# Kernel tuning notes

Measured on AMD Instinct MI355X. Metric: run time of the kernel, lower is better.

## Reference

```python
import jax, jax.numpy as jnp
import numpy as np

N = 4096        # n_nodes; must equal HID due to the model's mean(dim=1)->classifier quirk
IN_DIM = 512
HID = 4096
E = 65536       # N * avg_degree(16)


def _lin(k, out_dim, in_dim):
    return jax.random.normal(k, (out_dim, in_dim), jnp.float32) * 0.02


def setup_inputs() -> dict:
    key = jax.random.key(0)
    ks = jax.random.split(key, 8)
    return {
        "x": jax.random.normal(ks[0], (N, IN_DIM), jnp.float32),
        "edge_index": jax.random.randint(ks[1], (2, E), 0, N, dtype=jnp.int32),
        "W_embed": _lin(ks[2], HID, IN_DIM),
        "b_embed": jnp.zeros((HID,), jnp.float32),
        "W1": _lin(ks[3], HID, HID),
        "b1": jnp.zeros((HID,), jnp.float32),
        "W2": _lin(ks[4], HID, HID),
        "b2": jnp.zeros((HID,), jnp.float32),
        "Wc1": _lin(ks[5], HID // 2, HID),
        "bc1": jnp.zeros((HID // 2,), jnp.float32),
        "Wc2": _lin(ks[6], 1, HID // 2),
        "bc2": jnp.zeros((1,), jnp.float32),
    }


def reference(x, edge_index, W_embed, b_embed, W1, b1, W2, b2, Wc1, bc1, Wc2, bc2):
    row, col = edge_index[0], edge_index[1]
    # embed: Linear(in_dim, hidden)
    h = x @ W_embed.T + b_embed                       # [N, HID]
    # two GNN layers: gather neighbors, scatter-add, linear + relu
    for W, b in ((W1, b1), (W2, b2)):
        aggr = jax.ops.segment_sum(h[col], row, num_segments=h.shape[0])  # [N, HID]
        h = jax.nn.relu(aggr @ W.T + b)
    # faithful to original: mean over feature dim -> [N] (N == HID)
    hm = jnp.mean(h, axis=1)                          # [HID]
    z = jax.nn.relu(hm @ Wc1.T + bc1)                 # [HID//2]
    out = (z @ Wc2.T + bc2).squeeze(-1)               # scalar
    return out
```

## Files before the change

### kernel.cpp

```cpp
#include <hip/hip_runtime.h>
#include <hip/hip_bf16.h>


#define N_NODES 4096
#define IN_DIM_ 512
#define HID_ 4096
#define NEDGE 65536

typedef float f32x4 __attribute__((ext_vector_type(4)));
typedef float f32x2 __attribute__((ext_vector_type(2)));
typedef unsigned short u16x8 __attribute__((ext_vector_type(8)));
typedef int i32x8 __attribute__((ext_vector_type(8)));

#define ACT_SCALE 8.0f
#define W_SCALE 256.0f
#define G_SCALE 8.0f
#define G_STORE_MUL (8.0f / 2048.0f)

__device__ __forceinline__ unsigned short f2bf(float f) {
  unsigned u = __float_as_uint(f);
  return (unsigned short)((u + 0x7fffu + ((u >> 16) & 1u)) >> 16);
}
__device__ __forceinline__ float bf2f(unsigned short h) {
  return __uint_as_float((unsigned)h << 16);
}
__device__ __forceinline__ unsigned char f2fp8(float f) {
  int w = __builtin_amdgcn_cvt_pk_fp8_f32(f, f, 0, false);
  return (unsigned char)(w & 0xff);
}
__device__ __forceinline__ void fp8x4_acc(int w, float* acc) {
  f32x2 lo = __builtin_amdgcn_cvt_pk_f32_fp8(w, false);
  f32x2 hi = __builtin_amdgcn_cvt_pk_f32_fp8(w, true);
  acc[0] += lo[0]; acc[1] += lo[1]; acc[2] += hi[0]; acc[3] += hi[1];
}

__global__ __launch_bounds__(256) void cvt_fp8(const float* __restrict__ in,
                                               unsigned char* __restrict__ out,
                                               int n, float scale) {
  int i = (blockIdx.x * 256 + threadIdx.x) * 8;
  if (i >= n) return;
  const float4 a = *(const float4*)(in + i);
  const float4 b = *(const float4*)(in + i + 4);
  int w0 = __builtin_amdgcn_cvt_pk_fp8_f32(a.x * scale, a.y * scale, 0, false);
  w0 = __builtin_amdgcn_cvt_pk_fp8_f32(a.z * scale, a.w * scale, w0, true);
  int w1 = __builtin_amdgcn_cvt_pk_fp8_f32(b.x * scale, b.y * scale, 0, false);
  w1 = __builtin_amdgcn_cvt_pk_fp8_f32(b.z * scale, b.w * scale, w1, true);
  *(int2*)(out + i) = make_int2(w0, w1);
}

__global__ __launch_bounds__(256) void zero_i32(int* __restrict__ p, int n) {
  int i = blockIdx.x * 256 + threadIdx.x;
  if (i < n) p[i] = 0;
}

__global__ __launch_bounds__(256) void hist_rows(const int* __restrict__ row,
                                                 int* __restrict__ counts) {
  int e = blockIdx.x * 256 + threadIdx.x;
  if (e < NEDGE) atomicAdd(&counts[row[e]], 1);
}

__global__ __launch_bounds__(1024) void scan4096(const int* __restrict__ counts,
                                                 int* __restrict__ starts) {
  __shared__ int sa[1024], sb[1024];
  const int t = threadIdx.x;
  const int c0 = counts[t * 4], c1 = counts[t * 4 + 1],
            c2 = counts[t * 4 + 2], c3 = counts[t * 4 + 3];
  const int local = c0 + c1 + c2 + c3;
  sa[t] = local;
  __syncthreads();
  int* src = sa; int* dst = sb;
  for (int off = 1; off < 1024; off <<= 1) {
    int v = src[t];
    if (t >= off) v += src[t - off];
    dst[t] = v;
    __syncthreads();
    int* tmp = src; src = dst; dst = tmp;
  }
  const int excl = (t == 0) ? 0 : src[t - 1];
  starts[t * 4]     = excl;
  starts[t * 4 + 1] = excl + c0;
  starts[t * 4 + 2] = excl + c0 + c1;
  starts[t * 4 + 3] = excl + c0 + c1 + c2;
  if (t == 1023) starts[4096] = excl + local;
}

__global__ __launch_bounds__(256) void fill_adj(const int* __restrict__ row,
                                                const int* __restrict__ col,
                                                const int* __restrict__ starts,
                                                int* __restrict__ cursor,
                                                int* __restrict__ adj) {
  int e = blockIdx.x * 256 + threadIdx.x;
  if (e >= NEDGE) return;
  int r = row[e];
  int p = atomicAdd(&cursor[r], 1);
  adj[starts[r] + p] = col[e];
}

__device__ __forceinline__ i32x8 ld_frag(const char* base0) {
  const int4 lo = *(const int4*)(base0);
  const int4 hi = *(const int4*)(base0 + 8192);
  i32x8 f;
  f[0] = lo.x; f[1] = lo.y; f[2] = lo.z; f[3] = lo.w;
  f[4] = hi.x; f[5] = hi.y; f[6] = hi.z; f[7] = hi.w;
  return f;
}

__global__ __launch_bounds__(256) void gemm_mx(
    const unsigned char* __restrict__ A, const unsigned char* __restrict__ B,
    unsigned char* __restrict__ C, int N, int K,
    const float* __restrict__ bias, float mul) {
  __shared__ unsigned char As[128 * 128];
  __shared__ unsigned char Bs[128 * 128];
  const int t = threadIdx.x;
  const int bm = blockIdx.x * 128, bn = blockIdx.y * 128;
  const int wave = t >> 6, lane = t & 63;
  const int wm = (wave >> 1) * 64, wn = (wave & 1) * 64;
  const int m16 = lane & 15, quad = lane >> 4;

  f32x4 acc[4][4] = {};

  const int srow = t >> 2;
  const int sg = (t & 3) * 32;
  const unsigned char* Ag0 = A + (size_t)(bm + srow) * K + sg;
  const unsigned char* Ag1 = A + (size_t)(bm + 64 + srow) * K + sg;
  const unsigned char* Bg0 = B + (size_t)(bn + srow) * K + sg;
  const unsigned char* Bg1 = B + (size_t)(bn + 64 + srow) * K + sg;
  char* AsB = (char*)As;
  char* BsB = (char*)Bs;

#define GLDS(gp, lp)                                                       \
  __builtin_amdgcn_global_load_lds(                                        \
      (const __attribute__((address_space(1))) void*)(gp),                 \
      (__attribute__((address_space(3))) void*)(lp), 16, 0, 0)

  for (int kb = 0; kb < K; kb += 128) {
    GLDS(Ag0 + kb,      AsB + t * 16);
    GLDS(Ag1 + kb,      AsB + 4096 + t * 16);
    GLDS(Ag0 + kb + 16, AsB + 8192 + t * 16);
    GLDS(Ag1 + kb + 16, AsB + 12288 + t * 16);
    GLDS(Bg0 + kb,      BsB + t * 16);
    GLDS(Bg1 + kb,      BsB + 4096 + t * 16);
    GLDS(Bg0 + kb + 16, BsB + 8192 + t * 16);
    GLDS(Bg1 + kb + 16, BsB + 12288 + t * 16);
    __syncthreads();

    i32x8 af[4], bfr[4];
#pragma unroll
    for (int r = 0; r < 4; ++r)
      af[r] = ld_frag(AsB + (wm + r * 16 + m16) * 64 + quad * 16);
#pragma unroll
    for (int c = 0; c < 4; ++c)
      bfr[c] = ld_frag(BsB + (wn + c * 16 + m16) * 64 + quad * 16);
#pragma unroll
    for (int r = 0; r < 4; ++r)
#pragma unroll
      for (int c = 0; c < 4; ++c)
        acc[r][c] = __builtin_amdgcn_mfma_scale_f32_16x16x128_f8f6f4(
            af[r], bfr[c], acc[r][c], 0, 0,
            0, 0x7f7f7f7f, 0, 0x7f7f7f7f);
    __syncthreads();
  }
#undef GLDS

#pragma unroll
  for (int r = 0; r < 4; ++r) {
#pragma unroll
    for (int c = 0; c < 4; ++c) {
      const int row0 = bm + wm + r * 16 + quad * 4;
      const int col = bn + wn + c * 16 + m16;
      const float bv = bias ? ACT_SCALE * bias[col] : 0.0f;
#pragma unroll
      for (int i = 0; i < 4; ++i) {
        C[(size_t)(row0 + i) * N + col] = f2fp8(acc[r][c][i] * mul + bv);
      }
    }
  }
}

__global__ __launch_bounds__(256) void aggr_f8out(
    const unsigned char* __restrict__ g, const int* __restrict__ starts,
    const int* __restrict__ adj, const float* __restrict__ bias,
    unsigned char* __restrict__ hout) {
  const int node = blockIdx.y;
  const int f0 = blockIdx.x * 2048 + threadIdx.x * 8;
  float acc[8] = {0, 0, 0, 0, 0, 0, 0, 0};
  const int s = starts[node], e = starts[node + 1];
  int j = s;
  for (; j + 4 <= e; j += 4) {
    const int c0 = adj[j], c1 = adj[j + 1], c2 = adj[j + 2], c3 = adj[j + 3];
    int2 v0 = *(const int2*)(g + (size_t)c0 * HID_ + f0);
    int2 v1 = *(const int2*)(g + (size_t)c1 * HID_ + f0);
    int2 v2 = *(const int2*)(g + (size_t)c2 * HID_ + f0);
    int2 v3 = *(const int2*)(g + (size_t)c3 * HID_ + f0);
    fp8x4_acc(v0.x, acc);     fp8x4_acc(v0.y, acc + 4);
    fp8x4_acc(v1.x, acc);     fp8x4_acc(v1.y, acc + 4);
    fp8x4_acc(v2.x, acc);     fp8x4_acc(v2.y, acc + 4);
    fp8x4_acc(v3.x, acc);     fp8x4_acc(v3.y, acc + 4);
  }
  for (; j < e; ++j) {
    int2 v = *(const int2*)(g + (size_t)adj[j] * HID_ + f0);
    fp8x4_acc(v.x, acc);      fp8x4_acc(v.y, acc + 4);
  }
  const float4 b0 = *(const float4*)(bias + f0);
  const float4 b1 = *(const float4*)(bias + f0 + 4);
  const float bb[8] = {b0.x, b0.y, b0.z, b0.w, b1.x, b1.y, b1.z, b1.w};
  float v[8];
#pragma unroll
  for (int i = 0; i < 8; ++i)
    v[i] = ACT_SCALE * fmaxf(acc[i] * (1.0f / G_SCALE) + bb[i], 0.0f);
  int w0 = __builtin_amdgcn_cvt_pk_fp8_f32(v[0], v[1], 0, false);
  w0 = __builtin_amdgcn_cvt_pk_fp8_f32(v[2], v[3], w0, true);
  int w1 = __builtin_amdgcn_cvt_pk_fp8_f32(v[4], v[5], 0, false);
  w1 = __builtin_amdgcn_cvt_pk_fp8_f32(v[6], v[7], w1, true);
  *(int2*)(hout + (size_t)node * HID_ + f0) = make_int2(w0, w1);
}

__global__ __launch_bounds__(256) void aggr_bf16out(
    const unsigned char* __restrict__ g, const int* __restrict__ starts,
    const int* __restrict__ adj, const float* __restrict__ bias,
    unsigned short* __restrict__ hout) {
  const int node = blockIdx.y;
  const int f0 = blockIdx.x * 2048 + threadIdx.x * 8;
  float acc[8] = {0, 0, 0, 0, 0, 0, 0, 0};
  const int s = starts[node], e = starts[node + 1];
  int j = s;
  for (; j + 4 <= e; j += 4) {
    const int c0 = adj[j], c1 = adj[j + 1], c2 = adj[j + 2], c3 = adj[j + 3];
    int2 v0 = *(const int2*)(g + (size_t)c0 * HID_ + f0);
    int2 v1 = *(const int2*)(g + (size_t)c1 * HID_ + f0);
    int2 v2 = *(const int2*)(g + (size_t)c2 * HID_ + f0);
    int2 v3 = *(const int2*)(g + (size_t)c3 * HID_ + f0);
    fp8x4_acc(v0.x, acc);     fp8x4_acc(v0.y, acc + 4);
    fp8x4_acc(v1.x, acc);     fp8x4_acc(v1.y, acc + 4);
    fp8x4_acc(v2.x, acc);     fp8x4_acc(v2.y, acc + 4);
    fp8x4_acc(v3.x, acc);     fp8x4_acc(v3.y, acc + 4);
  }
  for (; j < e; ++j) {
    int2 v = *(const int2*)(g + (size_t)adj[j] * HID_ + f0);
    fp8x4_acc(v.x, acc);      fp8x4_acc(v.y, acc + 4);
  }
  const float4 b0 = *(const float4*)(bias + f0);
  const float4 b1 = *(const float4*)(bias + f0 + 4);
  const float bb[8] = {b0.x, b0.y, b0.z, b0.w, b1.x, b1.y, b1.z, b1.w};
  u16x8 r;
#pragma unroll
  for (int i = 0; i < 8; ++i)
    r[i] = f2bf(fmaxf(acc[i] * (1.0f / G_SCALE) + bb[i], 0.0f));
  *(u16x8*)(hout + (size_t)node * HID_ + f0) = r;
}

__global__ __launch_bounds__(256) void row_mean(const unsigned short* __restrict__ h,
                                                float* __restrict__ hm) {
  const int row = blockIdx.x, t = threadIdx.x;
  const u16x8* p = (const u16x8*)(h + (size_t)row * HID_);
  u16x8 v1 = p[t], v2 = p[t + 256];
  float s = 0.f;
#pragma unroll
  for (int i = 0; i < 8; ++i) s += bf2f(v1[i]) + bf2f(v2[i]);
  for (int off = 32; off > 0; off >>= 1) s += __shfl_down(s, off);
  __shared__ float ws[4];
  if ((t & 63) == 0) ws[t >> 6] = s;
  __syncthreads();
  if (t == 0) hm[row] = (ws[0] + ws[1] + ws[2] + ws[3]) * (1.0f / (float)HID_);
}

__global__ __launch_bounds__(256) void clf1(const float* __restrict__ Wc1,
                                            const float* __restrict__ bc1,
                                            const float* __restrict__ hm,
                                            float* __restrict__ z) {
  const int wave = threadIdx.x >> 6, lane = threadIdx.x & 63;
  const int j = blockIdx.x * 4 + wave;
  const float* w = Wc1 + (size_t)j * HID_;
  float s = 0.f;
  for (int i = lane; i < HID_; i += 64) s += w[i] * hm[i];
  for (int off = 32; off > 0; off >>= 1) s += __shfl_down(s, off);
  if (lane == 0) z[j] = fmaxf(s + bc1[j], 0.0f);
}

__global__ __launch_bounds__(256) void clf2(const float* __restrict__ Wc2,
                                            const float* __restrict__ bc2,
                                            const float* __restrict__ z,
                                            float* __restrict__ out) {
  const int t = threadIdx.x;
  float s = 0.f;
  for (int i = t; i < HID_ / 2; i += 256) s += z[i] * Wc2[i];
  for (int off = 32; off > 0; off >>= 1) s += __shfl_down(s, off);
  __shared__ float ws[4];
  if ((t & 63) == 0) ws[t >> 6] = s;
  __syncthreads();
  if (t == 0) out[0] = ws[0] + ws[1] + ws[2] + ws[3] + bc2[0];
}

extern "C" void kernel_launch(void* const* d_in, const int* in_sizes, int n_in,
                              void* d_out, int out_size, void* d_ws, size_t ws_size,
                              hipStream_t stream) {
  (void)in_sizes; (void)n_in; (void)out_size; (void)ws_size;
  const float* x       = (const float*)d_in[0];
  const int*   edge    = (const int*)d_in[1];
  const int*   row     = edge;
  const int*   col     = edge + NEDGE;
  const float* W_embed = (const float*)d_in[2];
  const float* b_embed = (const float*)d_in[3];
  const float* W1      = (const float*)d_in[4];
  const float* b1      = (const float*)d_in[5];
  const float* W2      = (const float*)d_in[6];
  const float* b2      = (const float*)d_in[7];
  const float* Wc1     = (const float*)d_in[8];
  const float* bc1     = (const float*)d_in[9];
  const float* Wc2     = (const float*)d_in[10];
  const float* bc2     = (const float*)d_in[11];
  float* out = (float*)d_out;

  char* ws = (char*)d_ws;
  size_t off = 0;
  auto alloc = [&](size_t bytes) {
    char* p = ws + off;
    off += (bytes + 255) & ~(size_t)255;
    return p;
  };
  unsigned char*  xf8  = (unsigned char*)alloc((size_t)N_NODES * IN_DIM_);
  unsigned char*  wef8 = (unsigned char*)alloc((size_t)HID_ * IN_DIM_);
  unsigned char*  w1f8 = (unsigned char*)alloc((size_t)HID_ * HID_);
  unsigned char*  w2f8 = (unsigned char*)alloc((size_t)HID_ * HID_);
  unsigned char*  h0f8 = (unsigned char*)alloc((size_t)N_NODES * HID_);
  unsigned char*  h1f8 = (unsigned char*)alloc((size_t)N_NODES * HID_);
  unsigned char*  g    = (unsigned char*)alloc((size_t)N_NODES * HID_);
  unsigned short* h2   = (unsigned short*)alloc((size_t)N_NODES * HID_ * 2);
  int* counts = (int*)alloc(N_NODES * 4);
  int* cursor = (int*)alloc(N_NODES * 4);
  int* starts = (int*)alloc((N_NODES + 1) * 4);
  int* adj    = (int*)alloc(NEDGE * 4);
  float* hm   = (float*)alloc(N_NODES * 4);
  float* z    = (float*)alloc((HID_ / 2) * 4);

  zero_i32<<<16, 256, 0, stream>>>(counts, N_NODES);
  zero_i32<<<16, 256, 0, stream>>>(cursor, N_NODES);
  hist_rows<<<NEDGE / 256, 256, 0, stream>>>(row, counts);
  scan4096<<<1, 1024, 0, stream>>>(counts, starts);
  fill_adj<<<NEDGE / 256, 256, 0, stream>>>(row, col, starts, cursor, adj);

  cvt_fp8<<<(N_NODES * IN_DIM_ / 8) / 256, 256, 0, stream>>>(x, xf8, N_NODES * IN_DIM_, ACT_SCALE);
  cvt_fp8<<<(HID_ * IN_DIM_ / 8) / 256, 256, 0, stream>>>(W_embed, wef8, HID_ * IN_DIM_, W_SCALE);
  cvt_fp8<<<(HID_ * HID_ / 8) / 256, 256, 0, stream>>>(W1, w1f8, HID_ * HID_, W_SCALE);
  cvt_fp8<<<(HID_ * HID_ / 8) / 256, 256, 0, stream>>>(W2, w2f8, HID_ * HID_, W_SCALE);

  gemm_mx<<<dim3(32, 32), 256, 0, stream>>>(xf8, wef8, h0f8, HID_, IN_DIM_,
                                            b_embed, G_STORE_MUL);
  gemm_mx<<<dim3(32, 32), 256, 0, stream>>>(h0f8, w1f8, g, HID_, HID_,
                                            nullptr, G_STORE_MUL);
  aggr_f8out<<<dim3(2, N_NODES), 256, 0, stream>>>(g, starts, adj, b1, h1f8);
  gemm_mx<<<dim3(32, 32), 256, 0, stream>>>(h1f8, w2f8, g, HID_, HID_,
                                            nullptr, G_STORE_MUL);
  aggr_bf16out<<<dim3(2, N_NODES), 256, 0, stream>>>(g, starts, adj, b2, h2);
  row_mean<<<N_NODES, 256, 0, stream>>>(h2, hm);
  clf1<<<(HID_ / 2) / 4, 256, 0, stream>>>(Wc1, bc1, hm, z);
  clf2<<<1, 256, 0, stream>>>(Wc2, bc2, z, out);
}
```

Baseline: 483.3 us.

## Fuse row-mean into second aggregation, merge conversions, classifiers, and zeroing

The second aggregation now reduces each node's ReLU output directly into the row mean with an atomicAdd, so the bf16 h2 buffer and the separate row_mean kernel are no longer needed. The four fp8 conversion launches become one, the two zeroing launches become one (it also clears hm and the output), and the two classifier kernels are fused by atomically accumulating z*Wc2 into the output. This cuts launch count and removes the write and re-read of a 32MB intermediate. In exchange, float atomics make the summation order nondeterministic.

```diff
diff --git a/kernel.cpp b/kernel.cpp
--- a/kernel.cpp
+++ b/kernel.cpp
@@ -9,7 +9,6 @@
 
 typedef float f32x4 __attribute__((ext_vector_type(4)));
 typedef float f32x2 __attribute__((ext_vector_type(2)));
-typedef unsigned short u16x8 __attribute__((ext_vector_type(8)));
 typedef int i32x8 __attribute__((ext_vector_type(8)));
 
 #define ACT_SCALE 8.0f
@@ -17,13 +16,6 @@
 #define G_SCALE 8.0f
 #define G_STORE_MUL (8.0f / 2048.0f)
 
-__device__ __forceinline__ unsigned short f2bf(float f) {
-  unsigned u = __float_as_uint(f);
-  return (unsigned short)((u + 0x7fffu + ((u >> 16) & 1u)) >> 16);
-}
-__device__ __forceinline__ float bf2f(unsigned short h) {
-  return __uint_as_float((unsigned)h << 16);
-}
 __device__ __forceinline__ unsigned char f2fp8(float f) {
   int w = __builtin_amdgcn_cvt_pk_fp8_f32(f, f, 0, false);
   return (unsigned char)(w & 0xff);
@@ -34,23 +26,32 @@
   acc[0] += lo[0]; acc[1] += lo[1]; acc[2] += hi[0]; acc[3] += hi[1];
 }
 
-__global__ __launch_bounds__(256) void cvt_fp8(const float* __restrict__ in,
-                                               unsigned char* __restrict__ out,
-                                               int n, float scale) {
-  int i = (blockIdx.x * 256 + threadIdx.x) * 8;
-  if (i >= n) return;
+__global__ __launch_bounds__(256) void zero_misc(int* __restrict__ p, int n,
+                                                 float* __restrict__ out) {
+  int i = blockIdx.x * 256 + threadIdx.x;
+  if (i < n) p[i] = 0;
+  if (i == 0) out[0] = 0.0f;
+}
+
+__global__ __launch_bounds__(256) void cvt_all(
+    const float* __restrict__ x, const float* __restrict__ we,
+    const float* __restrict__ w1, const float* __restrict__ w2,
+    unsigned char* __restrict__ xo, unsigned char* __restrict__ weo,
+    unsigned char* __restrict__ w1o, unsigned char* __restrict__ w2o) {
+  const int b = blockIdx.x;
+  const float* in; unsigned char* out; float scale; int base;
+  if (b < 1024)       { in = x;  out = xo;  scale = ACT_SCALE; base = b; }
+  else if (b < 2048)  { in = we; out = weo; scale = W_SCALE;   base = b - 1024; }
+  else if (b < 10240) { in = w1; out = w1o; scale = W_SCALE;   base = b - 2048; }
+  else                { in = w2; out = w2o; scale = W_SCALE;   base = b - 10240; }
+  const int i = (base * 256 + threadIdx.x) * 8;
   const float4 a = *(const float4*)(in + i);
-  const float4 b = *(const float4*)(in + i + 4);
+  const float4 c = *(const float4*)(in + i + 4);
   int w0 = __builtin_amdgcn_cvt_pk_fp8_f32(a.x * scale, a.y * scale, 0, false);
   w0 = __builtin_amdgcn_cvt_pk_fp8_f32(a.z * scale, a.w * scale, w0, true);
-  int w1 = __builtin_amdgcn_cvt_pk_fp8_f32(b.x * scale, b.y * scale, 0, false);
-  w1 = __builtin_amdgcn_cvt_pk_fp8_f32(b.z * scale, b.w * scale, w1, true);
-  *(int2*)(out + i) = make_int2(w0, w1);
-}
-
-__global__ __launch_bounds__(256) void zero_i32(int* __restrict__ p, int n) {
-  int i = blockIdx.x * 256 + threadIdx.x;
-  if (i < n) p[i] = 0;
+  int w1v = __builtin_amdgcn_cvt_pk_fp8_f32(c.x * scale, c.y * scale, 0, false);
+  w1v = __builtin_amdgcn_cvt_pk_fp8_f32(c.z * scale, c.w * scale, w1v, true);
+  *(int2*)(out + i) = make_int2(w0, w1v);
 }
 
 __global__ __launch_bounds__(256) void hist_rows(const int* __restrict__ row,
@@ -215,10 +216,10 @@
   *(int2*)(hout + (size_t)node * HID_ + f0) = make_int2(w0, w1);
 }
 
-__global__ __launch_bounds__(256) void aggr_bf16out(
+__global__ __launch_bounds__(256) void aggr_mean(
     const unsigned char* __restrict__ g, const int* __restrict__ starts,
     const int* __restrict__ adj, const float* __restrict__ bias,
-    unsigned short* __restrict__ hout) {
+    float* __restrict__ hm) {
   const int node = blockIdx.y;
   const int f0 = blockIdx.x * 2048 + threadIdx.x * 8;
   float acc[8] = {0, 0, 0, 0, 0, 0, 0, 0};
@@ -242,53 +243,35 @@
   const float4 b0 = *(const float4*)(bias + f0);
   const float4 b1 = *(const float4*)(bias + f0 + 4);
   const float bb[8] = {b0.x, b0.y, b0.z, b0.w, b1.x, b1.y, b1.z, b1.w};
-  u16x8 r;
+  float s8 = 0.f;
 #pragma unroll
   for (int i = 0; i < 8; ++i)
-    r[i] = f2bf(fmaxf(acc[i] * (1.0f / G_SCALE) + bb[i], 0.0f));
-  *(u16x8*)(hout + (size_t)node * HID_ + f0) = r;
-}
-
-__global__ __launch_bounds__(256) void row_mean(const unsigned short* __restrict__ h,
-                                                float* __restrict__ hm) {
-  const int row = blockIdx.x, t = threadIdx.x;
-  const u16x8* p = (const u16x8*)(h + (size_t)row * HID_);
-  u16x8 v1 = p[t], v2 = p[t + 256];
-  float s = 0.f;
-#pragma unroll
-  for (int i = 0; i < 8; ++i) s += bf2f(v1[i]) + bf2f(v2[i]);
-  for (int off = 32; off > 0; off >>= 1) s += __shfl_down(s, off);
+    s8 += fmaxf(acc[i] * (1.0f / G_SCALE) + bb[i], 0.0f);
+  for (int off = 32; off > 0; off >>= 1) s8 += __shfl_down(s8, off);
   __shared__ float ws[4];
-  if ((t & 63) == 0) ws[t >> 6] = s;
+  const int t = threadIdx.x;
+  if ((t & 63) == 0) ws[t >> 6] = s8;
   __syncthreads();
-  if (t == 0) hm[row] = (ws[0] + ws[1] + ws[2] + ws[3]) * (1.0f / (float)HID_);
-}
-
-__global__ __launch_bounds__(256) void clf1(const float* __restrict__ Wc1,
-                                            const float* __restrict__ bc1,
-                                            const float* __restrict__ hm,
-                                            float* __restrict__ z) {
+  if (t == 0)
+    atomicAdd(&hm[node], (ws[0] + ws[1] + ws[2] + ws[3]) * (1.0f / (float)HID_));
+}
+
+__global__ __launch_bounds__(256) void clf_fused(
+    const float* __restrict__ Wc1, const float* __restrict__ bc1,
+    const float* __restrict__ Wc2, const float* __restrict__ bc2,
+    const float* __restrict__ hm, float* __restrict__ out) {
   const int wave = threadIdx.x >> 6, lane = threadIdx.x & 63;
   const int j = blockIdx.x * 4 + wave;
   const float* w = Wc1 + (size_t)j * HID_;
   float s = 0.f;
   for (int i = lane; i < HID_; i += 64) s += w[i] * hm[i];
   for (int off = 32; off > 0; off >>= 1) s += __shfl_down(s, off);
-  if (lane == 0) z[j] = fmaxf(s + bc1[j], 0.0f);
-}
-
-__global__ __launch_bounds__(256) void clf2(const float* __restrict__ Wc2,
-                                            const float* __restrict__ bc2,
-                                            const float* __restrict__ z,
-                                            float* __restrict__ out) {
-  const int t = threadIdx.x;
-  float s = 0.f;
-  for (int i = t; i < HID_ / 2; i += 256) s += z[i] * Wc2[i];
-  for (int off = 32; off > 0; off >>= 1) s += __shfl_down(s, off);
-  __shared__ float ws[4];
-  if ((t & 63) == 0) ws[t >> 6] = s;
-  __syncthreads();
-  if (t == 0) out[0] = ws[0] + ws[1] + ws[2] + ws[3] + bc2[0];
+  if (lane == 0) {
+    float z = fmaxf(s + bc1[j], 0.0f);
+    float c = z * Wc2[j];
+    if (j == 0) c += bc2[0];
+    atomicAdd(out, c);
+  }
 }
 
 extern "C" void kernel_launch(void* const* d_in, const int* in_sizes, int n_in,
@@ -325,24 +308,17 @@
   unsigned char*  h0f8 = (unsigned char*)alloc((size_t)N_NODES * HID_);
   unsigned char*  h1f8 = (unsigned char*)alloc((size_t)N_NODES * HID_);
   unsigned char*  g    = (unsigned char*)alloc((size_t)N_NODES * HID_);
-  unsigned short* h2   = (unsigned short*)alloc((size_t)N_NODES * HID_ * 2);
-  int* counts = (int*)alloc(N_NODES * 4);
-  int* cursor = (int*)alloc(N_NODES * 4);
-  int* starts = (int*)alloc((N_NODES + 1) * 4);
-  int* adj    = (int*)alloc(NEDGE * 4);
-  float* hm   = (float*)alloc(N_NODES * 4);
-  float* z    = (float*)alloc((HID_ / 2) * 4);
-
-  zero_i32<<<16, 256, 0, stream>>>(counts, N_NODES);
-  zero_i32<<<16, 256, 0, stream>>>(cursor, N_NODES);
+  int*   counts = (int*)alloc(N_NODES * 4);
+  int*   cursor = (int*)alloc(N_NODES * 4);
+  float* hm     = (float*)alloc(N_NODES * 4);
+  int*   starts = (int*)alloc((N_NODES + 1) * 4);
+  int*   adj    = (int*)alloc(NEDGE * 4);
+
+  zero_misc<<<48, 256, 0, stream>>>(counts, 3 * N_NODES, out);
   hist_rows<<<NEDGE / 256, 256, 0, stream>>>(row, counts);
   scan4096<<<1, 1024, 0, stream>>>(counts, starts);
   fill_adj<<<NEDGE / 256, 256, 0, stream>>>(row, col, starts, cursor, adj);
-
-  cvt_fp8<<<(N_NODES * IN_DIM_ / 8) / 256, 256, 0, stream>>>(x, xf8, N_NODES * IN_DIM_, ACT_SCALE);
-  cvt_fp8<<<(HID_ * IN_DIM_ / 8) / 256, 256, 0, stream>>>(W_embed, wef8, HID_ * IN_DIM_, W_SCALE);
-  cvt_fp8<<<(HID_ * HID_ / 8) / 256, 256, 0, stream>>>(W1, w1f8, HID_ * HID_, W_SCALE);
-  cvt_fp8<<<(HID_ * HID_ / 8) / 256, 256, 0, stream>>>(W2, w2f8, HID_ * HID_, W_SCALE);
+  cvt_all<<<18432, 256, 0, stream>>>(x, W_embed, W1, W2, xf8, wef8, w1f8, w2f8);
 
   gemm_mx<<<dim3(32, 32), 256, 0, stream>>>(xf8, wef8, h0f8, HID_, IN_DIM_,
                                             b_embed, G_STORE_MUL);
@@ -351,8 +327,6 @@
   aggr_f8out<<<dim3(2, N_NODES), 256, 0, stream>>>(g, starts, adj, b1, h1f8);
   gemm_mx<<<dim3(32, 32), 256, 0, stream>>>(h1f8, w2f8, g, HID_, HID_,
                                             nullptr, G_STORE_MUL);
-  aggr_bf16out<<<dim3(2, N_NODES), 256, 0, stream>>>(g, starts, adj, b2, h2);
-  row_mean<<<N_NODES, 256, 0, stream>>>(h2, hm);
-  clf1<<<(HID_ / 2) / 4, 256, 0, stream>>>(Wc1, bc1, hm, z);
-  clf2<<<1, 256, 0, stream>>>(Wc2, bc2, z, out);
-}
+  aggr_mean<<<dim3(2, N_NODES), 256, 0, stream>>>(g, starts, adj, b2, hm);
+  clf_fused<<<(HID_ / 2) / 4, 256, 0, stream>>>(Wc1, bc1, Wc2, bc2, hm, out);
+}
```

After: 484.0 us. No clear change (+0.1%).
